# Optimization experiments

Hardware: AMD Instinct MI355X
Metric: run time of the kernel (lower is better)

## Reference

```python
import jax, jax.numpy as jnp
import numpy as np

N, IN_FEAT, OUT_FEAT = 16384, 1024, 4096


def setup_inputs() -> dict:
    key = jax.random.key(0)
    k_x, k_m, k_w, k_b = jax.random.split(key, 4)
    x = jax.random.normal(k_x, (N, IN_FEAT), dtype=jnp.float32)
    amask = jax.random.randint(k_m, (N,), 0, 2, dtype=jnp.int32)
    # nn.Linear(in_feat, out_feat): weight [out, in], bias [out]
    W = jax.random.normal(k_w, (OUT_FEAT, IN_FEAT), dtype=jnp.float32) * (1.0 / np.sqrt(IN_FEAT))
    b = jax.random.normal(k_b, (OUT_FEAT,), dtype=jnp.float32) * 0.001
    return {"x": x, "amask": amask, "W": W, "b": b}


def reference(x, amask, W, b):
    # Torch code gathers rows where amask != 0, applies linear (+identity act),
    # and scatters results back into a zero [N, out_feat] tensor. Equivalent
    # dense-math (jit-friendly, no data-dependent shapes): compute the linear
    # on all rows and zero out unmasked rows. Same output values.
    y = jnp.einsum('ni,oi->no', x, W) + b  # [N, out_feat]
    keep = (amask != 0)[:, None]
    return jnp.where(keep, y, jnp.zeros((), dtype=x.dtype))
```

## Files before the change

### kernel.cpp

```cpp
#include <hip/hip_runtime.h>
#include <hip/hip_bf16.h>
#include <stdint.h>

#define N_ROWS 16384
#define K_DIM  1024
#define N_OUT  4096

typedef __attribute__((ext_vector_type(8))) short short8;
typedef __attribute__((ext_vector_type(4))) float f32x4;
typedef __attribute__((ext_vector_type(4))) __bf16 bf16x4;

__global__ __launch_bounds__(1024) void prep_kernel(
    const int*   __restrict__ amask,
    const float* __restrict__ W,
    int* __restrict__ idx, int* __restrict__ zidx, int* __restrict__ count,
    __bf16* __restrict__ wb)
{
    const int t = threadIdx.x;
    if (blockIdx.x != 0) {
        const int i = (blockIdx.x - 1) * 1024 + t;
        float4 v = reinterpret_cast<const float4*>(W)[i];
        bf16x4 o;
        o[0] = (__bf16)v.x; o[1] = (__bf16)v.y; o[2] = (__bf16)v.z; o[3] = (__bf16)v.w;
        reinterpret_cast<bf16x4*>(wb)[i] = o;
        return;
    }
    __shared__ int sc[1024];
    const int base = t * 16;
    int mk[16];
#pragma unroll
    for (int g = 0; g < 4; ++g) {
        int4 m4 = reinterpret_cast<const int4*>(amask + base)[g];
        mk[g*4+0] = m4.x; mk[g*4+1] = m4.y; mk[g*4+2] = m4.z; mk[g*4+3] = m4.w;
    }
    int c = 0;
#pragma unroll
    for (int i = 0; i < 16; ++i) c += (mk[i] != 0) ? 1 : 0;
    int v = c;
    sc[t] = v;
    __syncthreads();
    for (int off = 1; off < 1024; off <<= 1) {
        int u = (t >= off) ? sc[t - off] : 0;
        __syncthreads();
        v += u; sc[t] = v;
        __syncthreads();
    }
    int b  = v - c;
    int zb = base - b;
#pragma unroll
    for (int i = 0; i < 16; ++i) {
        int r = base + i;
        if (mk[i] != 0) idx[b++] = r; else zidx[zb++] = r;
    }
    if (t == 1023) count[0] = v;
}

__global__ __launch_bounds__(256) void cvt_gather_kernel(
    const float* __restrict__ x, const int* __restrict__ idx,
    const int* __restrict__ count, __bf16* __restrict__ xb) {
    const int cnt = count[0];
    const int t = threadIdx.x;
    for (int j = blockIdx.x; j < cnt; j += gridDim.x) {
        const int row = idx[j];
        float4 v = reinterpret_cast<const float4*>(x + (size_t)row * K_DIM)[t];
        bf16x4 o;
        o[0] = (__bf16)v.x; o[1] = (__bf16)v.y; o[2] = (__bf16)v.z; o[3] = (__bf16)v.w;
        reinterpret_cast<bf16x4*>(xb + (size_t)j * K_DIM)[t] = o;
    }
}


#define GLL(SRC, DSTOFF)                                                       \
    __builtin_amdgcn_global_load_lds(                                          \
        (const __attribute__((address_space(1))) void*)(SRC),                  \
        (__attribute__((address_space(3))) void*)(ldsc + (DSTOFF)), 16, 0, 0)

__global__ __launch_bounds__(256) void gemm_kernel(
    const __bf16* __restrict__ A,
    const __bf16* __restrict__ B,
    const float*  __restrict__ bias,
    const int*    __restrict__ idx,
    const int*    __restrict__ zidx,
    const int*    __restrict__ count,
    float*        __restrict__ out)
{
    __shared__ short lds_all[8192];

    const int t  = threadIdx.x;
    const int l  = t & 63;
    const int w  = t >> 6;
    const int wm = w >> 1;
    const int wn = w & 1;

    const int cnt = count[0];
    const int aT  = (cnt + 127) >> 7;
    const int q   = (aT + 7) >> 3;

    const int bid = blockIdx.x;
    const int xcd = bid & 7;
    const int c   = bid >> 3;
    const int pre = min(xcd * q, aT);
    int own = aT - pre; if (own > q) own = q; if (own < 0) own = 0;
    const int h   = own * 32;

    const int hb   = (c * h) >> 9;
    const bool hvy = (((c + 1) * h) >> 9) > hb;

    if (!hvy) {
        const int tr    = (512 * xcd - 32 * pre) + (c - hb);
        const int ntriv = 4096 - aT * 32;
        const int nz    = N_ROWS - cnt;
        const int rpz   = (nz + ntriv - 1) / ntriv;
        const int lo    = tr * rpz;
        const int hi0   = lo + rpz;
        const int hi    = hi0 < nz ? hi0 : nz;
        const float4 zf = make_float4(0.f, 0.f, 0.f, 0.f);
        for (int i = lo + w; i < hi; i += 4) {
            const int row = zidx[i];
            float4* p = reinterpret_cast<float4*>(out + (size_t)row * N_OUT);
#pragma unroll
            for (int u = 0; u < 16; ++u)
                p[u * 64 + l] = zf;
        }
        return;
    }

    const int tm = pre + (hb % own);
    const int tn = hb / own;
    const int m0 = tm * 128;
    const int n0 = tn * 128;

    const int srow = t >> 2;
    const int sk8  = (t & 3) * 8;
    const __bf16* pA0 = A + (size_t)(m0 + srow) * K_DIM + sk8;
    const __bf16* pA1 = pA0 + (size_t)64 * K_DIM;
    const __bf16* pB0 = B + (size_t)(n0 + srow) * K_DIM + sk8;
    const __bf16* pB1 = pB0 + (size_t)64 * K_DIM;
    char* ldsc = (char*)lds_all;

    const int lr = l & 15;
    const int lk = (l >> 4) * 8;

    f32x4 acc[4][4] = {};

    for (int k0 = 0; k0 < K_DIM; k0 += 32) {
        GLL(pA0 + k0, t * 16);
        GLL(pA1 + k0, 4096 + t * 16);
        GLL(pB0 + k0, 8192 + t * 16);
        GLL(pB1 + k0, 12288 + t * 16);
        __syncthreads();

        short8 af[4], bf[4];
#pragma unroll
        for (int mi = 0; mi < 4; ++mi)
            af[mi] = *(const short8*)(lds_all + (wm*64 + mi*16 + lr)*32 + lk);
#pragma unroll
        for (int ni = 0; ni < 4; ++ni)
            bf[ni] = *(const short8*)(lds_all + 4096 + (wn*64 + ni*16 + lr)*32 + lk);

#pragma unroll
        for (int mi = 0; mi < 4; ++mi)
#pragma unroll
            for (int ni = 0; ni < 4; ++ni)
                acc[mi][ni] = __builtin_amdgcn_mfma_f32_16x16x32_bf16(
                    af[mi], bf[ni], acc[mi][ni], 0, 0, 0);
        __syncthreads();
    }

    const int lq = l >> 4;
    float bv[4];
#pragma unroll
    for (int ni = 0; ni < 4; ++ni) bv[ni] = bias[n0 + wn*64 + ni*16 + lr];

#pragma unroll
    for (int mi = 0; mi < 4; ++mi) {
        const int slot0 = m0 + wm*64 + mi*16 + lq*4;
        int rowid[4]; bool val[4];
#pragma unroll
        for (int r = 0; r < 4; ++r) {
            const int s = slot0 + r;
            val[r] = (s < cnt);
            rowid[r] = val[r] ? idx[s] : 0;
        }
#pragma unroll
        for (int ni = 0; ni < 4; ++ni) {
            const int cc = n0 + wn*64 + ni*16 + lr;
#pragma unroll
            for (int r = 0; r < 4; ++r)
                if (val[r]) out[(size_t)rowid[r] * N_OUT + cc] = acc[mi][ni][r] + bv[ni];
        }
    }
}

__global__ void naive_kernel(const float* __restrict__ x, const float* __restrict__ W,
                             const float* __restrict__ bias, const int* __restrict__ amask,
                             float* __restrict__ out) {
    int c = blockIdx.x * blockDim.x + threadIdx.x;
    int r = blockIdx.y;
    if (c >= N_OUT) return;
    if (amask[r] == 0) { out[(size_t)r * N_OUT + c] = 0.0f; return; }
    const float* xr = x + (size_t)r * K_DIM;
    const float* wr = W + (size_t)c * K_DIM;
    float s = 0.0f;
    for (int k = 0; k < K_DIM; ++k) s += xr[k] * wr[k];
    out[(size_t)r * N_OUT + c] = s + bias[c];
}

extern "C" void kernel_launch(void* const* d_in, const int* in_sizes, int n_in,
                              void* d_out, int out_size, void* d_ws, size_t ws_size,
                              hipStream_t stream) {
    const float* x     = (const float*)d_in[0];
    const int*   amask = (const int*)d_in[1];
    const float* W     = (const float*)d_in[2];
    const float* bias  = (const float*)d_in[3];
    float*       out   = (float*)d_out;

    const size_t xb_bytes = (size_t)N_ROWS * K_DIM * 2;
    const size_t wb_bytes = (size_t)N_OUT  * K_DIM * 2;
    const size_t idx_bytes = (size_t)N_ROWS * 4;
    const size_t need = xb_bytes + wb_bytes + 2 * idx_bytes + 256;

    if (ws_size < need) {
        dim3 g((N_OUT + 255) / 256, N_ROWS);
        naive_kernel<<<g, 256, 0, stream>>>(x, W, bias, amask, out);
        return;
    }

    __bf16* xb   = (__bf16*)d_ws;
    __bf16* wb   = (__bf16*)((char*)d_ws + xb_bytes);
    int*    idx  = (int*)((char*)d_ws + xb_bytes + wb_bytes);
    int*    zidx = idx + N_ROWS;
    int*    cnt  = zidx + N_ROWS;

    prep_kernel<<<1025, 1024, 0, stream>>>(amask, W, idx, zidx, cnt, wb);
    cvt_gather_kernel<<<2048, 256, 0, stream>>>(x, idx, cnt, xb);

    gemm_kernel<<<4096, 256, 0, stream>>>(xb, wb, bias, idx, zidx, cnt, out);
}
```

Measured before the change: 175.0 us.

## Move zero-fill of masked-out rows into gather kernel, simplify GEMM tile mapping

Zero-filling of rows whose mask is off moves out of the GEMM kernel and into the gather/convert kernel, which gains 1024 extra blocks for it. The GEMM now uses a plain blockIdx-to-tile mapping (tn = bid & 31, tm = bid >> 5), and blocks beyond the active M tiles exit early. This drops the XCD-aware interleaving of heavy GEMM tiles and trivial zero-fill work. In exchange the zero-fill no longer overlaps the GEMM, and the XCD-aware tile placement that may have helped L2 locality is lost.

```diff
diff --git a/kernel.cpp b/kernel.cpp
--- a/kernel.cpp
+++ b/kernel.cpp
@@ -55,17 +55,31 @@
     if (t == 1023) count[0] = v;
 }
 
-__global__ __launch_bounds__(256) void cvt_gather_kernel(
+__global__ __launch_bounds__(256) void gather_zfill_kernel(
     const float* __restrict__ x, const int* __restrict__ idx,
-    const int* __restrict__ count, __bf16* __restrict__ xb) {
-    const int cnt = count[0];
+    const int* __restrict__ zidx, const int* __restrict__ count,
+    __bf16* __restrict__ xb, float* __restrict__ out) {
     const int t = threadIdx.x;
-    for (int j = blockIdx.x; j < cnt; j += gridDim.x) {
-        const int row = idx[j];
-        float4 v = reinterpret_cast<const float4*>(x + (size_t)row * K_DIM)[t];
-        bf16x4 o;
-        o[0] = (__bf16)v.x; o[1] = (__bf16)v.y; o[2] = (__bf16)v.z; o[3] = (__bf16)v.w;
-        reinterpret_cast<bf16x4*>(xb + (size_t)j * K_DIM)[t] = o;
+    if (blockIdx.x < 2048) {
+        const int cnt = count[0];
+        for (int j = blockIdx.x; j < cnt; j += 2048) {
+            const int row = idx[j];
+            float4 v = reinterpret_cast<const float4*>(x + (size_t)row * K_DIM)[t];
+            bf16x4 o;
+            o[0] = (__bf16)v.x; o[1] = (__bf16)v.y; o[2] = (__bf16)v.z; o[3] = (__bf16)v.w;
+            reinterpret_cast<bf16x4*>(xb + (size_t)j * K_DIM)[t] = o;
+        }
+    } else {
+        const int nz = N_ROWS - count[0];
+        const int zb = blockIdx.x - 2048;
+        const float4 zf = make_float4(0.f, 0.f, 0.f, 0.f);
+        for (int i = zb; i < nz; i += 1024) {
+            const int row = zidx[i];
+            float4* p = reinterpret_cast<float4*>(out + (size_t)row * N_OUT);
+#pragma unroll
+            for (int u = 0; u < 4; ++u)
+                p[u * 256 + t] = zf;
+        }
     }
 }
 
@@ -80,11 +94,16 @@
     const __bf16* __restrict__ B,
     const float*  __restrict__ bias,
     const int*    __restrict__ idx,
-    const int*    __restrict__ zidx,
     const int*    __restrict__ count,
     float*        __restrict__ out)
 {
     __shared__ short lds_all[8192];
+
+    const int cnt = count[0];
+    const int aT  = (cnt + 127) >> 7;
+    const int tn  = blockIdx.x & 31;
+    const int tm  = blockIdx.x >> 5;
+    if (tm >= aT) return;
 
     const int t  = threadIdx.x;
     const int l  = t & 63;
@@ -92,41 +111,6 @@
     const int wm = w >> 1;
     const int wn = w & 1;
 
-    const int cnt = count[0];
-    const int aT  = (cnt + 127) >> 7;
-    const int q   = (aT + 7) >> 3;
-
-    const int bid = blockIdx.x;
-    const int xcd = bid & 7;
-    const int c   = bid >> 3;
-    const int pre = min(xcd * q, aT);
-    int own = aT - pre; if (own > q) own = q; if (own < 0) own = 0;
-    const int h   = own * 32;
-
-    const int hb   = (c * h) >> 9;
-    const bool hvy = (((c + 1) * h) >> 9) > hb;
-
-    if (!hvy) {
-        const int tr    = (512 * xcd - 32 * pre) + (c - hb);
-        const int ntriv = 4096 - aT * 32;
-        const int nz    = N_ROWS - cnt;
-        const int rpz   = (nz + ntriv - 1) / ntriv;
-        const int lo    = tr * rpz;
-        const int hi0   = lo + rpz;
-        const int hi    = hi0 < nz ? hi0 : nz;
-        const float4 zf = make_float4(0.f, 0.f, 0.f, 0.f);
-        for (int i = lo + w; i < hi; i += 4) {
-            const int row = zidx[i];
-            float4* p = reinterpret_cast<float4*>(out + (size_t)row * N_OUT);
-#pragma unroll
-            for (int u = 0; u < 16; ++u)
-                p[u * 64 + l] = zf;
-        }
-        return;
-    }
-
-    const int tm = pre + (hb % own);
-    const int tn = hb / own;
     const int m0 = tm * 128;
     const int n0 = tn * 128;
 
@@ -233,7 +217,6 @@
     int*    cnt  = zidx + N_ROWS;
 
     prep_kernel<<<1025, 1024, 0, stream>>>(amask, W, idx, zidx, cnt, wb);
-    cvt_gather_kernel<<<2048, 256, 0, stream>>>(x, idx, cnt, xb);
-
-    gemm_kernel<<<4096, 256, 0, stream>>>(xb, wb, bias, idx, zidx, cnt, out);
-}
+    gather_zfill_kernel<<<3072, 256, 0, stream>>>(x, idx, zidx, cnt, xb, out);
+    gemm_kernel<<<4096, 256, 0, stream>>>(xb, wb, bias, idx, cnt, out);
+}
```

Result: faster. 154.8 us (-11.5%).
